# Kernel optimization log

Measured on AMD Instinct MI355X. Metric: run time of the kernel, lower is better.

Reference implementation:

```python
import jax, jax.numpy as jnp
import numpy as np

N = 100          # node_num (pinned by linear2 in_features = 1000 = N*10)
F_IN = 27        # node_feature_size
E = 262144       # number of edges
EMB = 128        # embedding_size
BN_EPS = 1e-5


def gcn_conv(x, W, b, src, dst, ew):
    """PyG GCNConv with edge weights: symmetric norm + self loops (fill=1)."""
    xw = x @ W  # [N, out]
    deg = jax.ops.segment_sum(ew, dst, num_segments=N) + 1.0  # self-loop weight 1
    dinv = jnp.where(deg > 0, deg ** -0.5, 0.0)
    norm = dinv[src] * ew * dinv[dst]              # [E]
    msg = norm[:, None] * xw[src]                  # [E, out] gather + scale
    agg = jax.ops.segment_sum(msg, dst, num_segments=N)
    agg = agg + (dinv * dinv)[:, None] * xw        # self-loop contribution
    return agg + b


def setup_inputs() -> dict:
    key = jax.random.key(0)
    ks = jax.random.split(key, 16)
    def lin(k, fan_in, shape):
        bound = 1.0 / np.sqrt(fan_in)
        return jax.random.uniform(k, shape, jnp.float32, -bound, bound)
    return {
        "x": jax.random.normal(ks[0], (1, N, F_IN), jnp.float32),
        "edge_index": jax.random.randint(ks[1], (1, 2, E), 0, N, jnp.int32),
        "edge_attr": jax.random.uniform(ks[2], (1, E), jnp.float32),
        "W1": lin(ks[3], F_IN, (F_IN, 64)),  "b1": lin(ks[4], F_IN, (64,)),
        "W2": lin(ks[5], 64, (64, 128)),     "b2": lin(ks[6], 64, (128,)),
        "W3": lin(ks[7], 128, (128, 256)),   "b3": lin(ks[8], 128, (256,)),
        "gamma": jnp.ones((256,), jnp.float32), "beta": jnp.zeros((256,), jnp.float32),
        "lw1": lin(ks[9], 256, (10, 256)),   "lb1": lin(ks[10], 256, (10,)),
        "lw2": lin(ks[11], 1000, (EMB, 1000)), "lb2": lin(ks[12], 1000, (EMB,)),
    }


def reference(x, edge_index, edge_attr, W1, b1, W2, b2, W3, b3,
              gamma, beta, lw1, lb1, lw2, lb2):
    h = x[0].reshape(N, -1)
    src, dst = edge_index[0, 0], edge_index[0, 1]
    ew = edge_attr[0]
    h = jax.nn.relu(gcn_conv(h, W1, b1, src, dst, ew))
    h = jax.nn.relu(gcn_conv(h, W2, b2, src, dst, ew))
    h = jax.nn.relu(gcn_conv(h, W3, b3, src, dst, ew))
    # BatchNorm1d (training-mode batch stats, biased var)
    mu = jnp.mean(h, axis=0)
    var = jnp.mean((h - mu) ** 2, axis=0)
    h = (h - mu) * jax.lax.rsqrt(var + BN_EPS) * gamma + beta
    # scatter_max with index=arange(N) is the identity permutation -> no-op
    h = (h @ lw1.T + lb1).reshape(-1)  # [N*10] = [1000]
    h = jax.nn.relu(h)
    return h @ lw2.T + lb2             # [EMB]
```

## Files before the change

### kernel.cpp

```cpp
#include <hip/hip_runtime.h>

#define NN 100
#define EE 262144
#define NP 16

#define WS_D   160000
#define WS_MS  161600
#define WS_H2  162112
#define WS_H3  174912

__global__ __launch_bounds__(1024) void scatter_kernel(
    const int* __restrict__ ei, const float* __restrict__ ew,
    float* __restrict__ P, float* __restrict__ D, float* __restrict__ MS)
{
    __shared__ float hist[NN * NN];
    __shared__ float part[NN][4];
    const int tid = threadIdx.x, blk = blockIdx.x;
    for (int i = tid; i < 2500; i += 1024)
        ((float4*)hist)[i] = make_float4(0.f, 0.f, 0.f, 0.f);
    if (blk == 0 && tid < 128)
        ((float4*)MS)[tid] = make_float4(0.f, 0.f, 0.f, 0.f);
    __syncthreads();
    const int base = blk * 4096;
#pragma unroll
    for (int it = 0; it < 4; ++it) {
        int q = base + it * 1024 + tid;
        int4   s4 = ((const int4*)ei)[q];
        int4   d4 = ((const int4*)(ei + EE))[q];
        float4 w4 = ((const float4*)ew)[q];
        atomicAdd(&hist[d4.x * NN + s4.x], w4.x);
        atomicAdd(&hist[d4.y * NN + s4.y], w4.y);
        atomicAdd(&hist[d4.z * NN + s4.z], w4.z);
        atomicAdd(&hist[d4.w * NN + s4.w], w4.w);
    }
    __syncthreads();
    for (int i = tid; i < 2500; i += 1024)
        ((float4*)(P + blk * 10000))[i] = ((const float4*)hist)[i];
    if (tid < 400) {
        int row = tid >> 2, q = tid & 3;
        const float* r = hist + row * NN + q * 25;
        float s = 0.f;
#pragma unroll
        for (int k = 0; k < 25; ++k) s += r[k];
        part[row][q] = s;
    }
    __syncthreads();
    if (tid < NN)
        D[blk * NN + tid] = part[tid][0] + part[tid][1] + part[tid][2] + part[tid][3];
}

__global__ __launch_bounds__(256) void mid1_kernel(
    const float* __restrict__ P, const float* __restrict__ D,
    const float* __restrict__ x,
    const float* __restrict__ W1, const float* __restrict__ b1,
    const float* __restrict__ W2, const float* __restrict__ b2,
    float* __restrict__ h2g)
{
    __shared__ float A[NN * NN];
    __shared__ float xl[NN * 28];
    __shared__ float g1[NN * 28];
    __shared__ float W1l[27 * 64];
    __shared__ float b1l[64];
    __shared__ float h1l[NN * 64];
    __shared__ float dv[NN];
    __shared__ float g2[64];
    const int tid = threadIdx.x, d = blockIdx.x;

    for (int i = tid; i < NN * 28; i += 256) {
        int n = i / 28, c = i - n * 28;
        xl[i] = (c < 27) ? x[n * 27 + c] : 0.f;
    }
    for (int i = tid; i < 27 * 64; i += 256) W1l[i] = W1[i];
    if (tid < 64) b1l[tid] = b1[tid];
    if (tid < NN) {
        float deg = 1.f;
#pragma unroll
        for (int p = 0; p < NP; ++p) deg += D[p * NN + tid];
        dv[tid] = rsqrtf(deg);
    }
    __syncthreads();

    for (int i4 = tid; i4 < 2500; i4 += 256) {
        float4 s = ((const float4*)P)[i4];
#pragma unroll
        for (int p = 1; p < NP; ++p) {
            float4 b = ((const float4*)P)[p * 2500 + i4];
            s.x += b.x; s.y += b.y; s.z += b.z; s.w += b.w;
        }
        int r = i4 / 25, c0 = (i4 - r * 25) * 4;
        float dr = dv[r], dd = dr * dr;
        float4 a;
        a.x = dr * dv[c0 + 0] * s.x; if (r == c0 + 0) a.x += dd;
        a.y = dr * dv[c0 + 1] * s.y; if (r == c0 + 1) a.y += dd;
        a.z = dr * dv[c0 + 2] * s.z; if (r == c0 + 2) a.z += dd;
        a.w = dr * dv[c0 + 3] * s.w; if (r == c0 + 3) a.w += dd;
        ((float4*)A)[i4] = a;
    }
    __syncthreads();

    if (tid < 175) {
        int nt = tid / 7, n0 = nt * 4, c0 = (tid - nt * 7) * 4;
        float acc[4][4];
#pragma unroll
        for (int r = 0; r < 4; ++r)
#pragma unroll
            for (int q = 0; q < 4; ++q) acc[r][q] = 0.f;
        for (int m = 0; m < NN; m += 4) {
            float4 a0 = *(const float4*)(A + (n0 + 0) * NN + m);
            float4 a1 = *(const float4*)(A + (n0 + 1) * NN + m);
            float4 a2 = *(const float4*)(A + (n0 + 2) * NN + m);
            float4 a3 = *(const float4*)(A + (n0 + 3) * NN + m);
            float4 x0 = *(const float4*)(xl + (m + 0) * 28 + c0);
            float4 x1 = *(const float4*)(xl + (m + 1) * 28 + c0);
            float4 x2 = *(const float4*)(xl + (m + 2) * 28 + c0);
            float4 x3 = *(const float4*)(xl + (m + 3) * 28 + c0);
#define GROW(r, ar) \
            acc[r][0] += ar.x*x0.x + ar.y*x1.x + ar.z*x2.x + ar.w*x3.x; \
            acc[r][1] += ar.x*x0.y + ar.y*x1.y + ar.z*x2.y + ar.w*x3.y; \
            acc[r][2] += ar.x*x0.z + ar.y*x1.z + ar.z*x2.z + ar.w*x3.z; \
            acc[r][3] += ar.x*x0.w + ar.y*x1.w + ar.z*x2.w + ar.w*x3.w;
            GROW(0, a0) GROW(1, a1) GROW(2, a2) GROW(3, a3)
#undef GROW
        }
#pragma unroll
        for (int r = 0; r < 4; ++r)
            *(float4*)(g1 + (n0 + r) * 28 + c0) =
                make_float4(acc[r][0], acc[r][1], acc[r][2], acc[r][3]);
    }
    __syncthreads();

    for (int t = tid; t < 400; t += 256) {
        int nt = t / 16, n0 = nt * 4, j0 = (t - nt * 16) * 4;
        float acc[4][4];
#pragma unroll
        for (int r = 0; r < 4; ++r)
#pragma unroll
            for (int q = 0; q < 4; ++q) acc[r][q] = 0.f;
        for (int c = 0; c < 24; c += 4) {
            float4 w0 = *(const float4*)(W1l + (c + 0) * 64 + j0);
            float4 w1 = *(const float4*)(W1l + (c + 1) * 64 + j0);
            float4 w2 = *(const float4*)(W1l + (c + 2) * 64 + j0);
            float4 w3 = *(const float4*)(W1l + (c + 3) * 64 + j0);
            float4 g0 = *(const float4*)(g1 + (n0 + 0) * 28 + c);
            float4 g1_ = *(const float4*)(g1 + (n0 + 1) * 28 + c);
            float4 g2_ = *(const float4*)(g1 + (n0 + 2) * 28 + c);
            float4 g3_ = *(const float4*)(g1 + (n0 + 3) * 28 + c);
#define TROW(r, gr) \
            acc[r][0] += gr.x*w0.x + gr.y*w1.x + gr.z*w2.x + gr.w*w3.x; \
            acc[r][1] += gr.x*w0.y + gr.y*w1.y + gr.z*w2.y + gr.w*w3.y; \
            acc[r][2] += gr.x*w0.z + gr.y*w1.z + gr.z*w2.z + gr.w*w3.z; \
            acc[r][3] += gr.x*w0.w + gr.y*w1.w + gr.z*w2.w + gr.w*w3.w;
            TROW(0, g0) TROW(1, g1_) TROW(2, g2_) TROW(3, g3_)
#undef TROW
        }
#pragma unroll
        for (int c = 24; c < 27; ++c) {
            float4 wq = *(const float4*)(W1l + c * 64 + j0);
#pragma unroll
            for (int r = 0; r < 4; ++r) {
                float gv = g1[(n0 + r) * 28 + c];
                acc[r][0] += gv * wq.x; acc[r][1] += gv * wq.y;
                acc[r][2] += gv * wq.z; acc[r][3] += gv * wq.w;
            }
        }
        float4 bq = *(const float4*)(b1l + j0);
#pragma unroll
        for (int r = 0; r < 4; ++r) {
            float4 v;
            v.x = fmaxf(acc[r][0] + bq.x, 0.f); v.y = fmaxf(acc[r][1] + bq.y, 0.f);
            v.z = fmaxf(acc[r][2] + bq.z, 0.f); v.w = fmaxf(acc[r][3] + bq.w, 0.f);
            *(float4*)(h1l + (n0 + r) * 64 + j0) = v;
        }
    }
    __syncthreads();

    if (tid < 64) {
        const float* Ar = A + d * NN;
        float acc = 0.f;
#pragma unroll 4
        for (int m = 0; m < NN; ++m) acc += Ar[m] * h1l[m * 64 + tid];
        g2[tid] = acc;
    }
    __syncthreads();

    if (tid < 128) {
        float acc = b2[tid];
#pragma unroll 8
        for (int c = 0; c < 64; ++c) acc += g2[c] * W2[c * 128 + tid];
        h2g[d * 128 + tid] = fmaxf(acc, 0.f);
    }
}

__global__ __launch_bounds__(256) void l3_kernel(
    const float* __restrict__ P, const float* __restrict__ D,
    const float* __restrict__ h2g,
    const float* __restrict__ W3, const float* __restrict__ b3,
    float* __restrict__ h3g, float* __restrict__ MS)
{
    __shared__ float h2l[NN * 128];
    __shared__ float dv[NN];
    __shared__ float Ar[NN];
    __shared__ float g3[128];
    const int tid = threadIdx.x, d = blockIdx.x;

    for (int i = tid; i < NN * 32; i += 256)
        ((float4*)h2l)[i] = ((const float4*)h2g)[i];
    if (tid < NN) {
        float deg = 1.f;
#pragma unroll
        for (int p = 0; p < NP; ++p) deg += D[p * NN + tid];
        dv[tid] = rsqrtf(deg);
    }
    __syncthreads();
    if (tid < NN) {
        float s = 0.f;
#pragma unroll
        for (int p = 0; p < NP; ++p) s += P[p * 10000 + d * NN + tid];
        float v = dv[d] * dv[tid] * s;
        if (tid == d) v += dv[d] * dv[d];
        Ar[tid] = v;
    }
    __syncthreads();
    if (tid < 128) {
        float acc = 0.f;
#pragma unroll 4
        for (int m = 0; m < NN; ++m) acc += Ar[m] * h2l[m * 128 + tid];
        g3[tid] = acc;
    }
    __syncthreads();
    {
        int j = tid;
        float acc = b3[j];
#pragma unroll 8
        for (int c = 0; c < 128; ++c) acc += g3[c] * W3[c * 256 + j];
        float v = fmaxf(acc, 0.f);
        h3g[d * 256 + j] = v;
        atomicAdd(&MS[j], v);
        atomicAdd(&MS[256 + j], v * v);
    }
}

__global__ __launch_bounds__(256) void tail_kernel(
    const float* __restrict__ h3g, const float* __restrict__ MS,
    const float* __restrict__ gamma, const float* __restrict__ beta,
    const float* __restrict__ lw1, const float* __restrict__ lb1,
    const float* __restrict__ lw2, const float* __restrict__ lb2,
    float* __restrict__ out)
{
    __shared__ float sc[256], sh[256];
    __shared__ float wsc[2560];
    __shared__ float cst[10];
    __shared__ float yl[1000];
    __shared__ float partw[4];
    const int tid = threadIdx.x, j = blockIdx.x;

    {
        float s1 = MS[tid], s2 = MS[256 + tid];
        float mu  = s1 * 0.01f;
        float var = s2 * 0.01f - mu * mu;
        float s   = gamma[tid] * rsqrtf(var + 1e-5f);
        sc[tid] = s;
        sh[tid] = beta[tid] - mu * s;
    }
    __syncthreads();
    for (int i = tid; i < 2560; i += 256) wsc[i] = sc[i & 255] * lw1[i];
    if (tid < 10) {
        float a = lb1[tid];
        const float* w = lw1 + tid * 256;
#pragma unroll 4
        for (int c = 0; c < 256; ++c) a += sh[c] * w[c];
        cst[tid] = a;
    }
    __syncthreads();

    if (tid < 250) {
        int n0 = (tid / 5) * 2, k0 = (tid % 5) * 2;
        float a00 = 0.f, a01 = 0.f, a10 = 0.f, a11 = 0.f;
        for (int c = 0; c < 256; c += 4) {
            float4 hA = *(const float4*)(h3g + n0 * 256 + c);
            float4 hB = *(const float4*)(h3g + (n0 + 1) * 256 + c);
            float4 wA = *(const float4*)(wsc + k0 * 256 + c);
            float4 wB = *(const float4*)(wsc + (k0 + 1) * 256 + c);
            a00 += hA.x*wA.x + hA.y*wA.y + hA.z*wA.z + hA.w*wA.w;
            a01 += hA.x*wB.x + hA.y*wB.y + hA.z*wB.z + hA.w*wB.w;
            a10 += hB.x*wA.x + hB.y*wA.y + hB.z*wA.z + hB.w*wA.w;
            a11 += hB.x*wB.x + hB.y*wB.y + hB.z*wB.z + hB.w*wB.w;
        }
        yl[n0 * 10 + k0]           = fmaxf(a00 + cst[k0], 0.f);
        yl[n0 * 10 + k0 + 1]       = fmaxf(a01 + cst[k0 + 1], 0.f);
        yl[(n0 + 1) * 10 + k0]     = fmaxf(a10 + cst[k0], 0.f);
        yl[(n0 + 1) * 10 + k0 + 1] = fmaxf(a11 + cst[k0 + 1], 0.f);
    }
    __syncthreads();

    float acc = 0.f;
    if (tid < 250) {
        float4 a = ((const float4*)yl)[tid];
        float4 b = ((const float4*)(lw2 + j * 1000))[tid];
        acc = a.x * b.x + a.y * b.y + a.z * b.z + a.w * b.w;
    }
#pragma unroll
    for (int off = 32; off; off >>= 1) acc += __shfl_down(acc, off);
    if ((tid & 63) == 0) partw[tid >> 6] = acc;
    __syncthreads();
    if (tid == 0)
        out[j] = partw[0] + partw[1] + partw[2] + partw[3] + lb2[j];
}

extern "C" void kernel_launch(void* const* d_in, const int* in_sizes, int n_in,
                              void* d_out, int out_size, void* d_ws, size_t ws_size,
                              hipStream_t stream) {
    const float* x     = (const float*)d_in[0];
    const int*   ei    = (const int*)d_in[1];
    const float* ew    = (const float*)d_in[2];
    const float* W1    = (const float*)d_in[3];
    const float* b1    = (const float*)d_in[4];
    const float* W2    = (const float*)d_in[5];
    const float* b2    = (const float*)d_in[6];
    const float* W3    = (const float*)d_in[7];
    const float* b3    = (const float*)d_in[8];
    const float* gamma = (const float*)d_in[9];
    const float* beta  = (const float*)d_in[10];
    const float* lw1   = (const float*)d_in[11];
    const float* lb1   = (const float*)d_in[12];
    const float* lw2   = (const float*)d_in[13];
    const float* lb2   = (const float*)d_in[14];

    float* ws  = (float*)d_ws;
    float* P   = ws;
    float* D   = ws + WS_D;
    float* MS  = ws + WS_MS;
    float* h2  = ws + WS_H2;
    float* h3  = ws + WS_H3;
    float* out = (float*)d_out;

    scatter_kernel<<<NP, 1024, 0, stream>>>(ei, ew, P, D, MS);
    mid1_kernel<<<NN, 256, 0, stream>>>(P, D, x, W1, b1, W2, b2, h2);
    l3_kernel<<<NN, 256, 0, stream>>>(P, D, h2, W3, b3, h3, MS);
    tail_kernel<<<128, 256, 0, stream>>>(h3, MS, gamma, beta, lw1, lb1,
                                         lw2, lb2, out);
}
```

Measured before the change: 158.9 us.

## Fuse GCN layers and tail into one persistent kernel with grid barriers

Replaces the three post-scatter kernels with one 128-block persistent kernel that separates stages with software grid barriers, removing two kernel launches and their gaps. The scatter now runs on 64 blocks of 512 threads instead of 16 of 1024, for more parallelism in the histogram phase. The 64 partial histograms are reduced once per row and stored to a shared global sum, and degrees are taken from those row sums. The cost is spin-wait barriers that assume all 128 blocks are co-resident, plus a larger partial-sum reduction.

```diff
diff --git a/kernel.cpp b/kernel.cpp
--- a/kernel.cpp
+++ b/kernel.cpp
@@ -2,29 +2,36 @@
 
 #define NN 100
 #define EE 262144
-#define NP 16
-
-#define WS_D   160000
-#define WS_MS  161600
-#define WS_H2  162112
-#define WS_H3  174912
-
-__global__ __launch_bounds__(1024) void scatter_kernel(
+#define NSC 64
+#define NB2 128
+#define NT2 256
+
+#define WS_D    640000
+#define WS_MS   646400
+#define WS_BAR  646912
+#define WS_SS   646928
+#define WS_DEG  656928
+#define WS_H2   657028
+#define WS_H3   669828
+
+__global__ __launch_bounds__(512) void scatter_kernel(
     const int* __restrict__ ei, const float* __restrict__ ew,
-    float* __restrict__ P, float* __restrict__ D, float* __restrict__ MS)
+    float* __restrict__ P, float* __restrict__ D,
+    float* __restrict__ MS, int* __restrict__ bar)
 {
     __shared__ float hist[NN * NN];
     __shared__ float part[NN][4];
     const int tid = threadIdx.x, blk = blockIdx.x;
-    for (int i = tid; i < 2500; i += 1024)
+    for (int i = tid; i < 2500; i += 512)
         ((float4*)hist)[i] = make_float4(0.f, 0.f, 0.f, 0.f);
-    if (blk == 0 && tid < 128)
-        ((float4*)MS)[tid] = make_float4(0.f, 0.f, 0.f, 0.f);
-    __syncthreads();
-    const int base = blk * 4096;
-#pragma unroll
-    for (int it = 0; it < 4; ++it) {
-        int q = base + it * 1024 + tid;
+    if (blk == 0) {
+        if (tid < 128) ((float4*)MS)[tid] = make_float4(0.f, 0.f, 0.f, 0.f);
+        if (tid >= 128 && tid < 144) bar[tid - 128] = 0;
+    }
+    __syncthreads();
+    const int base = blk * 1024;
+#pragma unroll
+    for (int q = base + tid; q < base + 1024; q += 512) {
         int4   s4 = ((const int4*)ei)[q];
         int4   d4 = ((const int4*)(ei + EE))[q];
         float4 w4 = ((const float4*)ew)[q];
@@ -34,7 +41,7 @@
         atomicAdd(&hist[d4.w * NN + s4.w], w4.w);
     }
     __syncthreads();
-    for (int i = tid; i < 2500; i += 1024)
+    for (int i = tid; i < 2500; i += 512)
         ((float4*)(P + blk * 10000))[i] = ((const float4*)hist)[i];
     if (tid < 400) {
         int row = tid >> 2, q = tid & 3;
@@ -49,262 +56,284 @@
         D[blk * NN + tid] = part[tid][0] + part[tid][1] + part[tid][2] + part[tid][3];
 }
 
-__global__ __launch_bounds__(256) void mid1_kernel(
-    const float* __restrict__ P, const float* __restrict__ D,
+__device__ __forceinline__ void gridbar(int* bar, int k) {
+    __threadfence();
+    __syncthreads();
+    if (threadIdx.x == 0) {
+        atomicAdd(&bar[k], 1);
+        for (int it = 0; it < (1 << 22); ++it) {
+            if (__hip_atomic_load(&bar[k], __ATOMIC_RELAXED,
+                                  __HIP_MEMORY_SCOPE_AGENT) >= NB2) break;
+            __builtin_amdgcn_s_sleep(1);
+        }
+        __threadfence();
+    }
+    __syncthreads();
+}
+
+__global__ __launch_bounds__(NT2) void mega_kernel(
     const float* __restrict__ x,
     const float* __restrict__ W1, const float* __restrict__ b1,
     const float* __restrict__ W2, const float* __restrict__ b2,
-    float* __restrict__ h2g)
-{
-    __shared__ float A[NN * NN];
-    __shared__ float xl[NN * 28];
-    __shared__ float g1[NN * 28];
-    __shared__ float W1l[27 * 64];
-    __shared__ float b1l[64];
-    __shared__ float h1l[NN * 64];
-    __shared__ float dv[NN];
-    __shared__ float g2[64];
-    const int tid = threadIdx.x, d = blockIdx.x;
-
-    for (int i = tid; i < NN * 28; i += 256) {
-        int n = i / 28, c = i - n * 28;
-        xl[i] = (c < 27) ? x[n * 27 + c] : 0.f;
-    }
-    for (int i = tid; i < 27 * 64; i += 256) W1l[i] = W1[i];
-    if (tid < 64) b1l[tid] = b1[tid];
-    if (tid < NN) {
-        float deg = 1.f;
-#pragma unroll
-        for (int p = 0; p < NP; ++p) deg += D[p * NN + tid];
-        dv[tid] = rsqrtf(deg);
-    }
-    __syncthreads();
-
-    for (int i4 = tid; i4 < 2500; i4 += 256) {
-        float4 s = ((const float4*)P)[i4];
-#pragma unroll
-        for (int p = 1; p < NP; ++p) {
-            float4 b = ((const float4*)P)[p * 2500 + i4];
-            s.x += b.x; s.y += b.y; s.z += b.z; s.w += b.w;
-        }
-        int r = i4 / 25, c0 = (i4 - r * 25) * 4;
-        float dr = dv[r], dd = dr * dr;
-        float4 a;
-        a.x = dr * dv[c0 + 0] * s.x; if (r == c0 + 0) a.x += dd;
-        a.y = dr * dv[c0 + 1] * s.y; if (r == c0 + 1) a.y += dd;
-        a.z = dr * dv[c0 + 2] * s.z; if (r == c0 + 2) a.z += dd;
-        a.w = dr * dv[c0 + 3] * s.w; if (r == c0 + 3) a.w += dd;
-        ((float4*)A)[i4] = a;
-    }
-    __syncthreads();
-
-    if (tid < 175) {
-        int nt = tid / 7, n0 = nt * 4, c0 = (tid - nt * 7) * 4;
-        float acc[4][4];
-#pragma unroll
-        for (int r = 0; r < 4; ++r)
-#pragma unroll
-            for (int q = 0; q < 4; ++q) acc[r][q] = 0.f;
-        for (int m = 0; m < NN; m += 4) {
-            float4 a0 = *(const float4*)(A + (n0 + 0) * NN + m);
-            float4 a1 = *(const float4*)(A + (n0 + 1) * NN + m);
-            float4 a2 = *(const float4*)(A + (n0 + 2) * NN + m);
-            float4 a3 = *(const float4*)(A + (n0 + 3) * NN + m);
-            float4 x0 = *(const float4*)(xl + (m + 0) * 28 + c0);
-            float4 x1 = *(const float4*)(xl + (m + 1) * 28 + c0);
-            float4 x2 = *(const float4*)(xl + (m + 2) * 28 + c0);
-            float4 x3 = *(const float4*)(xl + (m + 3) * 28 + c0);
-#define GROW(r, ar) \
-            acc[r][0] += ar.x*x0.x + ar.y*x1.x + ar.z*x2.x + ar.w*x3.x; \
-            acc[r][1] += ar.x*x0.y + ar.y*x1.y + ar.z*x2.y + ar.w*x3.y; \
-            acc[r][2] += ar.x*x0.z + ar.y*x1.z + ar.z*x2.z + ar.w*x3.z; \
-            acc[r][3] += ar.x*x0.w + ar.y*x1.w + ar.z*x2.w + ar.w*x3.w;
-            GROW(0, a0) GROW(1, a1) GROW(2, a2) GROW(3, a3)
-#undef GROW
-        }
-#pragma unroll
-        for (int r = 0; r < 4; ++r)
-            *(float4*)(g1 + (n0 + r) * 28 + c0) =
-                make_float4(acc[r][0], acc[r][1], acc[r][2], acc[r][3]);
-    }
-    __syncthreads();
-
-    for (int t = tid; t < 400; t += 256) {
-        int nt = t / 16, n0 = nt * 4, j0 = (t - nt * 16) * 4;
-        float acc[4][4];
-#pragma unroll
-        for (int r = 0; r < 4; ++r)
-#pragma unroll
-            for (int q = 0; q < 4; ++q) acc[r][q] = 0.f;
-        for (int c = 0; c < 24; c += 4) {
-            float4 w0 = *(const float4*)(W1l + (c + 0) * 64 + j0);
-            float4 w1 = *(const float4*)(W1l + (c + 1) * 64 + j0);
-            float4 w2 = *(const float4*)(W1l + (c + 2) * 64 + j0);
-            float4 w3 = *(const float4*)(W1l + (c + 3) * 64 + j0);
-            float4 g0 = *(const float4*)(g1 + (n0 + 0) * 28 + c);
-            float4 g1_ = *(const float4*)(g1 + (n0 + 1) * 28 + c);
-            float4 g2_ = *(const float4*)(g1 + (n0 + 2) * 28 + c);
-            float4 g3_ = *(const float4*)(g1 + (n0 + 3) * 28 + c);
-#define TROW(r, gr) \
-            acc[r][0] += gr.x*w0.x + gr.y*w1.x + gr.z*w2.x + gr.w*w3.x; \
-            acc[r][1] += gr.x*w0.y + gr.y*w1.y + gr.z*w2.y + gr.w*w3.y; \
-            acc[r][2] += gr.x*w0.z + gr.y*w1.z + gr.z*w2.z + gr.w*w3.z; \
-            acc[r][3] += gr.x*w0.w + gr.y*w1.w + gr.z*w2.w + gr.w*w3.w;
-            TROW(0, g0) TROW(1, g1_) TROW(2, g2_) TROW(3, g3_)
-#undef TROW
-        }
-#pragma unroll
-        for (int c = 24; c < 27; ++c) {
-            float4 wq = *(const float4*)(W1l + c * 64 + j0);
-#pragma unroll
-            for (int r = 0; r < 4; ++r) {
-                float gv = g1[(n0 + r) * 28 + c];
-                acc[r][0] += gv * wq.x; acc[r][1] += gv * wq.y;
-                acc[r][2] += gv * wq.z; acc[r][3] += gv * wq.w;
-            }
-        }
-        float4 bq = *(const float4*)(b1l + j0);
-#pragma unroll
-        for (int r = 0; r < 4; ++r) {
-            float4 v;
-            v.x = fmaxf(acc[r][0] + bq.x, 0.f); v.y = fmaxf(acc[r][1] + bq.y, 0.f);
-            v.z = fmaxf(acc[r][2] + bq.z, 0.f); v.w = fmaxf(acc[r][3] + bq.w, 0.f);
-            *(float4*)(h1l + (n0 + r) * 64 + j0) = v;
-        }
-    }
-    __syncthreads();
-
-    if (tid < 64) {
-        const float* Ar = A + d * NN;
-        float acc = 0.f;
-#pragma unroll 4
-        for (int m = 0; m < NN; ++m) acc += Ar[m] * h1l[m * 64 + tid];
-        g2[tid] = acc;
-    }
-    __syncthreads();
-
-    if (tid < 128) {
-        float acc = b2[tid];
-#pragma unroll 8
-        for (int c = 0; c < 64; ++c) acc += g2[c] * W2[c * 128 + tid];
-        h2g[d * 128 + tid] = fmaxf(acc, 0.f);
-    }
-}
-
-__global__ __launch_bounds__(256) void l3_kernel(
-    const float* __restrict__ P, const float* __restrict__ D,
-    const float* __restrict__ h2g,
     const float* __restrict__ W3, const float* __restrict__ b3,
-    float* __restrict__ h3g, float* __restrict__ MS)
-{
-    __shared__ float h2l[NN * 128];
-    __shared__ float dv[NN];
-    __shared__ float Ar[NN];
-    __shared__ float g3[128];
-    const int tid = threadIdx.x, d = blockIdx.x;
-
-    for (int i = tid; i < NN * 32; i += 256)
-        ((float4*)h2l)[i] = ((const float4*)h2g)[i];
-    if (tid < NN) {
-        float deg = 1.f;
-#pragma unroll
-        for (int p = 0; p < NP; ++p) deg += D[p * NN + tid];
-        dv[tid] = rsqrtf(deg);
-    }
-    __syncthreads();
-    if (tid < NN) {
-        float s = 0.f;
-#pragma unroll
-        for (int p = 0; p < NP; ++p) s += P[p * 10000 + d * NN + tid];
-        float v = dv[d] * dv[tid] * s;
-        if (tid == d) v += dv[d] * dv[d];
-        Ar[tid] = v;
-    }
-    __syncthreads();
-    if (tid < 128) {
-        float acc = 0.f;
-#pragma unroll 4
-        for (int m = 0; m < NN; ++m) acc += Ar[m] * h2l[m * 128 + tid];
-        g3[tid] = acc;
-    }
-    __syncthreads();
-    {
-        int j = tid;
-        float acc = b3[j];
-#pragma unroll 8
-        for (int c = 0; c < 128; ++c) acc += g3[c] * W3[c * 256 + j];
-        float v = fmaxf(acc, 0.f);
-        h3g[d * 256 + j] = v;
-        atomicAdd(&MS[j], v);
-        atomicAdd(&MS[256 + j], v * v);
-    }
-}
-
-__global__ __launch_bounds__(256) void tail_kernel(
-    const float* __restrict__ h3g, const float* __restrict__ MS,
     const float* __restrict__ gamma, const float* __restrict__ beta,
     const float* __restrict__ lw1, const float* __restrict__ lb1,
     const float* __restrict__ lw2, const float* __restrict__ lb2,
-    float* __restrict__ out)
+    float* __restrict__ ws, float* __restrict__ out)
 {
-    __shared__ float sc[256], sh[256];
-    __shared__ float wsc[2560];
-    __shared__ float cst[10];
-    __shared__ float yl[1000];
-    __shared__ float partw[4];
-    const int tid = threadIdx.x, j = blockIdx.x;
+    __shared__ float lds[24000];
+    float* P    = ws;
+    float* D    = ws + WS_D;
+    float* MS   = ws + WS_MS;
+    int*   bar  = (int*)(ws + WS_BAR);
+    float* Ssum = ws + WS_SS;
+    float* degg = ws + WS_DEG;
+    float* h2g  = ws + WS_H2;
+    float* h3g  = ws + WS_H3;
+    const int tid = threadIdx.x, blk = blockIdx.x;
+
+    if (blk < NN) {
+        float* row = lds + 10000;
+        if (tid < NN) {
+            float s = 0.f;
+#pragma unroll 8
+            for (int p = 0; p < NSC; ++p) s += P[p * 10000 + blk * NN + tid];
+            row[tid] = s;
+            Ssum[blk * NN + tid] = s;
+        }
+        float dsum = 0.f;
+        if (tid < NN) {
+            float dd = 0.f;
+#pragma unroll
+            for (int p = 0; p < NSC; ++p) dd += D[p * NN + tid];
+            dsum = dd;
+        }
+        __syncthreads();
+        if (tid == 0) {
+            float deg = 1.f;
+            for (int i = 0; i < NN; ++i) deg += row[i];
+            degg[blk] = deg;
+        }
+        (void)dsum;
+    }
+    gridbar(bar, 0);
+
+    float* A = lds;
+    if (blk < NN) {
+        float* xl  = lds + 10000;
+        float* g1  = lds + 12800;
+        float* W1l = lds + 15600;
+        float* b1l = lds + 17328;
+        float* dv  = lds + 17392;
+        float* h1l = lds + 17492;
+        float* g2  = lds + 23892;
+        const int d = blk;
+
+        for (int i = tid; i < NN * 28; i += NT2) {
+            int n = i / 28, c = i - n * 28;
+            xl[i] = (c < 27) ? x[n * 27 + c] : 0.f;
+        }
+        for (int i = tid; i < 27 * 64; i += NT2) W1l[i] = W1[i];
+        if (tid < 64) b1l[tid] = b1[tid];
+        if (tid < NN) dv[tid] = rsqrtf(degg[tid]);
+        __syncthreads();
+
+        for (int i4 = tid; i4 < 2500; i4 += NT2) {
+            float4 s = ((const float4*)Ssum)[i4];
+            int r = i4 / 25, c0 = (i4 - r * 25) * 4;
+            float dr = dv[r], dd2 = dr * dr;
+            float4 a;
+            a.x = dr * dv[c0 + 0] * s.x; if (r == c0 + 0) a.x += dd2;
+            a.y = dr * dv[c0 + 1] * s.y; if (r == c0 + 1) a.y += dd2;
+            a.z = dr * dv[c0 + 2] * s.z; if (r == c0 + 2) a.z += dd2;
+            a.w = dr * dv[c0 + 3] * s.w; if (r == c0 + 3) a.w += dd2;
+            ((float4*)A)[i4] = a;
+        }
+        __syncthreads();
+
+        if (tid < 175) {
+            int nt = tid / 7, n0 = nt * 4, c0 = (tid - nt * 7) * 4;
+            float acc[4][4];
+#pragma unroll
+            for (int r = 0; r < 4; ++r)
+#pragma unroll
+                for (int q = 0; q < 4; ++q) acc[r][q] = 0.f;
+            for (int m = 0; m < NN; m += 4) {
+                float4 a0 = *(const float4*)(A + (n0 + 0) * NN + m);
+                float4 a1 = *(const float4*)(A + (n0 + 1) * NN + m);
+                float4 a2 = *(const float4*)(A + (n0 + 2) * NN + m);
+                float4 a3 = *(const float4*)(A + (n0 + 3) * NN + m);
+                float4 x0 = *(const float4*)(xl + (m + 0) * 28 + c0);
+                float4 x1 = *(const float4*)(xl + (m + 1) * 28 + c0);
+                float4 x2 = *(const float4*)(xl + (m + 2) * 28 + c0);
+                float4 x3 = *(const float4*)(xl + (m + 3) * 28 + c0);
+#define GROW(r, ar) \
+                acc[r][0] += ar.x*x0.x + ar.y*x1.x + ar.z*x2.x + ar.w*x3.x; \
+                acc[r][1] += ar.x*x0.y + ar.y*x1.y + ar.z*x2.y + ar.w*x3.y; \
+                acc[r][2] += ar.x*x0.z + ar.y*x1.z + ar.z*x2.z + ar.w*x3.z; \
+                acc[r][3] += ar.x*x0.w + ar.y*x1.w + ar.z*x2.w + ar.w*x3.w;
+                GROW(0, a0) GROW(1, a1) GROW(2, a2) GROW(3, a3)
+#undef GROW
+            }
+#pragma unroll
+            for (int r = 0; r < 4; ++r)
+                *(float4*)(g1 + (n0 + r) * 28 + c0) =
+                    make_float4(acc[r][0], acc[r][1], acc[r][2], acc[r][3]);
+        }
+        __syncthreads();
+
+        for (int t = tid; t < 400; t += NT2) {
+            int nt = t / 16, n0 = nt * 4, j0 = (t - nt * 16) * 4;
+            float acc[4][4];
+#pragma unroll
+            for (int r = 0; r < 4; ++r)
+#pragma unroll
+                for (int q = 0; q < 4; ++q) acc[r][q] = 0.f;
+            for (int c = 0; c < 24; c += 4) {
+                float4 w0 = *(const float4*)(W1l + (c + 0) * 64 + j0);
+                float4 w1 = *(const float4*)(W1l + (c + 1) * 64 + j0);
+                float4 w2 = *(const float4*)(W1l + (c + 2) * 64 + j0);
+                float4 w3 = *(const float4*)(W1l + (c + 3) * 64 + j0);
+                float4 g0 = *(const float4*)(g1 + (n0 + 0) * 28 + c);
+                float4 g1_ = *(const float4*)(g1 + (n0 + 1) * 28 + c);
+                float4 g2_ = *(const float4*)(g1 + (n0 + 2) * 28 + c);
+                float4 g3_ = *(const float4*)(g1 + (n0 + 3) * 28 + c);
+#define TROW(r, gr) \
+                acc[r][0] += gr.x*w0.x + gr.y*w1.x + gr.z*w2.x + gr.w*w3.x; \
+                acc[r][1] += gr.x*w0.y + gr.y*w1.y + gr.z*w2.y + gr.w*w3.y; \
+                acc[r][2] += gr.x*w0.z + gr.y*w1.z + gr.z*w2.z + gr.w*w3.z; \
+                acc[r][3] += gr.x*w0.w + gr.y*w1.w + gr.z*w2.w + gr.w*w3.w;
+                TROW(0, g0) TROW(1, g1_) TROW(2, g2_) TROW(3, g3_)
+#undef TROW
+            }
+#pragma unroll
+            for (int c = 24; c < 27; ++c) {
+                float4 wq = *(const float4*)(W1l + c * 64 + j0);
+#pragma unroll
+                for (int r = 0; r < 4; ++r) {
+                    float gv = g1[(n0 + r) * 28 + c];
+                    acc[r][0] += gv * wq.x; acc[r][1] += gv * wq.y;
+                    acc[r][2] += gv * wq.z; acc[r][3] += gv * wq.w;
+                }
+            }
+            float4 bq = *(const float4*)(b1l + j0);
+#pragma unroll
+            for (int r = 0; r < 4; ++r) {
+                float4 v;
+                v.x = fmaxf(acc[r][0] + bq.x, 0.f); v.y = fmaxf(acc[r][1] + bq.y, 0.f);
+                v.z = fmaxf(acc[r][2] + bq.z, 0.f); v.w = fmaxf(acc[r][3] + bq.w, 0.f);
+                *(float4*)(h1l + (n0 + r) * 64 + j0) = v;
+            }
+        }
+        __syncthreads();
+
+        if (tid < 64) {
+            const float* Ar = A + d * NN;
+            float acc = 0.f;
+#pragma unroll 4
+            for (int m = 0; m < NN; ++m) acc += Ar[m] * h1l[m * 64 + tid];
+            g2[tid] = acc;
+        }
+        __syncthreads();
+
+        if (tid < 128) {
+            float acc = b2[tid];
+#pragma unroll 8
+            for (int c = 0; c < 64; ++c) acc += g2[c] * W2[c * 128 + tid];
+            h2g[d * 128 + tid] = fmaxf(acc, 0.f);
+        }
+    }
+    gridbar(bar, 1);
+
+    if (blk < NN) {
+        float* h2l = lds + 10000;
+        float* g3  = lds + 22800;
+        const int d = blk;
+        for (int i = tid; i < NN * 32; i += NT2)
+            ((float4*)h2l)[i] = ((const float4*)h2g)[i];
+        __syncthreads();
+        if (tid < 128) {
+            const float* Ar = A + d * NN;
+            float acc = 0.f;
+#pragma unroll 4
+            for (int m = 0; m < NN; ++m) acc += Ar[m] * h2l[m * 128 + tid];
+            g3[tid] = acc;
+        }
+        __syncthreads();
+        {
+            int j = tid;
+            float acc = b3[j];
+#pragma unroll 8
+            for (int c = 0; c < 128; ++c) acc += g3[c] * W3[c * 256 + j];
+            float v = fmaxf(acc, 0.f);
+            h3g[d * 256 + j] = v;
+            atomicAdd(&MS[j], v);
+            atomicAdd(&MS[256 + j], v * v);
+        }
+    }
+    gridbar(bar, 2);
 
     {
-        float s1 = MS[tid], s2 = MS[256 + tid];
-        float mu  = s1 * 0.01f;
-        float var = s2 * 0.01f - mu * mu;
-        float s   = gamma[tid] * rsqrtf(var + 1e-5f);
-        sc[tid] = s;
-        sh[tid] = beta[tid] - mu * s;
-    }
-    __syncthreads();
-    for (int i = tid; i < 2560; i += 256) wsc[i] = sc[i & 255] * lw1[i];
-    if (tid < 10) {
-        float a = lb1[tid];
-        const float* w = lw1 + tid * 256;
+        float* sc   = lds;
+        float* sh   = lds + 256;
+        float* wsc  = lds + 512;
+        float* cst  = lds + 3072;
+        float* yl   = lds + 3082;
+        float* partw= lds + 4082;
+        const int j = blk;
+
+        {
+            float s1 = MS[tid], s2 = MS[256 + tid];
+            float mu  = s1 * 0.01f;
+            float var = s2 * 0.01f - mu * mu;
+            float s   = gamma[tid] * rsqrtf(var + 1e-5f);
+            sc[tid] = s;
+            sh[tid] = beta[tid] - mu * s;
+        }
+        __syncthreads();
+        for (int i = tid; i < 2560; i += NT2) wsc[i] = sc[i & 255] * lw1[i];
+        if (tid < 10) {
+            float a = lb1[tid];
+            const float* w = lw1 + tid * 256;
 #pragma unroll 4
-        for (int c = 0; c < 256; ++c) a += sh[c] * w[c];
-        cst[tid] = a;
-    }
-    __syncthreads();
-
-    if (tid < 250) {
-        int n0 = (tid / 5) * 2, k0 = (tid % 5) * 2;
-        float a00 = 0.f, a01 = 0.f, a10 = 0.f, a11 = 0.f;
-        for (int c = 0; c < 256; c += 4) {
-            float4 hA = *(const float4*)(h3g + n0 * 256 + c);
-            float4 hB = *(const float4*)(h3g + (n0 + 1) * 256 + c);
-            float4 wA = *(const float4*)(wsc + k0 * 256 + c);
-            float4 wB = *(const float4*)(wsc + (k0 + 1) * 256 + c);
-            a00 += hA.x*wA.x + hA.y*wA.y + hA.z*wA.z + hA.w*wA.w;
-            a01 += hA.x*wB.x + hA.y*wB.y + hA.z*wB.z + hA.w*wB.w;
-            a10 += hB.x*wA.x + hB.y*wA.y + hB.z*wA.z + hB.w*wA.w;
-            a11 += hB.x*wB.x + hB.y*wB.y + hB.z*wB.z + hB.w*wB.w;
-        }
-        yl[n0 * 10 + k0]           = fmaxf(a00 + cst[k0], 0.f);
-        yl[n0 * 10 + k0 + 1]       = fmaxf(a01 + cst[k0 + 1], 0.f);
-        yl[(n0 + 1) * 10 + k0]     = fmaxf(a10 + cst[k0], 0.f);
-        yl[(n0 + 1) * 10 + k0 + 1] = fmaxf(a11 + cst[k0 + 1], 0.f);
-    }
-    __syncthreads();
-
-    float acc = 0.f;
-    if (tid < 250) {
-        float4 a = ((const float4*)yl)[tid];
-        float4 b = ((const float4*)(lw2 + j * 1000))[tid];
-        acc = a.x * b.x + a.y * b.y + a.z * b.z + a.w * b.w;
-    }
-#pragma unroll
-    for (int off = 32; off; off >>= 1) acc += __shfl_down(acc, off);
-    if ((tid & 63) == 0) partw[tid >> 6] = acc;
-    __syncthreads();
-    if (tid == 0)
-        out[j] = partw[0] + partw[1] + partw[2] + partw[3] + lb2[j];
+            for (int c = 0; c < 256; ++c) a += sh[c] * w[c];
+            cst[tid] = a;
+        }
+        __syncthreads();
+
+        if (tid < 250) {
+            int n0 = (tid / 5) * 2, k0 = (tid % 5) * 2;
+            float a00 = 0.f, a01 = 0.f, a10 = 0.f, a11 = 0.f;
+            for (int c = 0; c < 256; c += 4) {
+                float4 hA = *(const float4*)(h3g + n0 * 256 + c);
+                float4 hB = *(const float4*)(h3g + (n0 + 1) * 256 + c);
+                float4 wA = *(const float4*)(wsc + k0 * 256 + c);
+                float4 wB = *(const float4*)(wsc + (k0 + 1) * 256 + c);
+                a00 += hA.x*wA.x + hA.y*wA.y + hA.z*wA.z + hA.w*wA.w;
+                a01 += hA.x*wB.x + hA.y*wB.y + hA.z*wB.z + hA.w*wB.w;
+                a10 += hB.x*wA.x + hB.y*wA.y + hB.z*wA.z + hB.w*wA.w;
+                a11 += hB.x*wB.x + hB.y*wB.y + hB.z*wB.z + hB.w*wB.w;
+            }
+            yl[n0 * 10 + k0]           = fmaxf(a00 + cst[k0], 0.f);
+            yl[n0 * 10 + k0 + 1]       = fmaxf(a01 + cst[k0 + 1], 0.f);
+            yl[(n0 + 1) * 10 + k0]     = fmaxf(a10 + cst[k0], 0.f);
+            yl[(n0 + 1) * 10 + k0 + 1] = fmaxf(a11 + cst[k0 + 1], 0.f);
+        }
+        __syncthreads();
+
+        float acc = 0.f;
+        if (tid < 250) {
+            float4 a = ((const float4*)yl)[tid];
+            float4 b = ((const float4*)(lw2 + j * 1000))[tid];
+            acc = a.x * b.x + a.y * b.y + a.z * b.z + a.w * b.w;
+        }
+#pragma unroll
+        for (int off = 32; off; off >>= 1) acc += __shfl_down(acc, off);
+        if ((tid & 63) == 0) partw[tid >> 6] = acc;
+        __syncthreads();
+        if (tid == 0)
+            out[j] = partw[0] + partw[1] + partw[2] + partw[3] + lb2[j];
+    }
 }
 
 extern "C" void kernel_launch(void* const* d_in, const int* in_sizes, int n_in,
@@ -327,16 +356,11 @@
     const float* lb2   = (const float*)d_in[14];
 
     float* ws  = (float*)d_ws;
-    float* P   = ws;
-    float* D   = ws + WS_D;
-    float* MS  = ws + WS_MS;
-    float* h2  = ws + WS_H2;
-    float* h3  = ws + WS_H3;
     float* out = (float*)d_out;
 
-    scatter_kernel<<<NP, 1024, 0, stream>>>(ei, ew, P, D, MS);
-    mid1_kernel<<<NN, 256, 0, stream>>>(P, D, x, W1, b1, W2, b2, h2);
-    l3_kernel<<<NN, 256, 0, stream>>>(P, D, h2, W3, b3, h3, MS);
-    tail_kernel<<<128, 256, 0, stream>>>(h3, MS, gamma, beta, lw1, lb1,
-                                         lw2, lb2, out);
+    scatter_kernel<<<NSC, 512, 0, stream>>>(ei, ew, ws, ws + WS_D,
+                                            ws + WS_MS, (int*)(ws + WS_BAR));
+    mega_kernel<<<NB2, NT2, 0, stream>>>(x, W1, b1, W2, b2, W3, b3,
+                                         gamma, beta, lw1, lb1, lw2, lb2,
+                                         ws, out);
 }
```

Result: slower. 174.0 us (+9.5%).
